# Performance work log

Measured on AMD Instinct MI355X. Metric: run time of the kernel, lower is better.

## Reference

```python
import jax, jax.numpy as jnp
import numpy as np

B, S, IN, D, H, L, DFF, C = 64, 256, 32, 512, 8, 2, 2048, 16
DH = D // H


def setup_inputs() -> dict:
    key = jax.random.key(0)
    ks = iter(jax.random.split(key, 40))
    r = lambda shp, s=0.02: (jax.random.normal(next(ks), shp, dtype=jnp.float32) * s)
    inp = {
        'x': jax.random.normal(next(ks), (B, S, IN), dtype=jnp.float32),
        'W_emb': r((IN, D)), 'b_emb': jnp.zeros((D,), jnp.float32),
        'Wq': r((L, D, D)), 'bq': jnp.zeros((L, D), jnp.float32),
        'Wk': r((L, D, D)), 'bk': jnp.zeros((L, D), jnp.float32),
        'Wv': r((L, D, D)), 'bv': jnp.zeros((L, D), jnp.float32),
        'Wo': r((L, D, D)), 'bo': jnp.zeros((L, D), jnp.float32),
        'ln1_s': jnp.ones((L, D), jnp.float32), 'ln1_b': jnp.zeros((L, D), jnp.float32),
        'W1': r((L, D, DFF)), 'b1': jnp.zeros((L, DFF), jnp.float32),
        'W2': r((L, DFF, D)), 'b2': jnp.zeros((L, D), jnp.float32),
        'ln2_s': jnp.ones((L, D), jnp.float32), 'ln2_b': jnp.zeros((L, D), jnp.float32),
        'e1_w': r((D, 128)), 'e1_b': jnp.zeros((128,), jnp.float32),
        'e2_w': r((128, D)), 'e2_b': jnp.zeros((D,), jnp.float32),
        'd1_w': r((D, 128)), 'd1_b': jnp.zeros((128,), jnp.float32),
        'd2_w': r((128, D)), 'd2_b': jnp.zeros((D,), jnp.float32),
        'y': jax.random.randint(next(ks), (B, S, 1), 0, C, dtype=jnp.int32),
    }
    return inp


def _ln(x, s, b):
    m = x.mean(-1, keepdims=True)
    v = ((x - m) ** 2).mean(-1, keepdims=True)
    return (x - m) / jnp.sqrt(v + 1e-5) * s + b


def _ari(a, t, n_cls):
    # adjusted rand index from contingency matrix (labels in [0, n_cls))
    idx = a * n_cls + t
    cm = jnp.zeros((n_cls * n_cls,), jnp.float32).at[idx].add(1.0).reshape(n_cls, n_cls)
    comb2 = lambda m: m * (m - 1.0) * 0.5
    sij = comb2(cm).sum()
    sa = comb2(cm.sum(1)).sum()
    sb = comb2(cm.sum(0)).sum()
    n = jnp.float32(a.shape[0])
    exp = sa * sb / (n * (n - 1.0) * 0.5)
    mx = 0.5 * (sa + sb)
    return (sij - exp) / (mx - exp)


def _net(x, W_emb, b_emb, Wq, bq, Wk, bk, Wv, bv, Wo, bo, ln1_s, ln1_b,
         W1, b1, W2, b2, ln2_s, ln2_b, e1_w, e1_b, e2_w, e2_b, d1_w, d1_b, d2_w, d2_b):
    h = x @ W_emb + b_emb  # [B,S,D]
    for l in range(L):
        q = (h @ Wq[l] + bq[l]).reshape(B, S, H, DH)
        k = (h @ Wk[l] + bk[l]).reshape(B, S, H, DH)
        v = (h @ Wv[l] + bv[l]).reshape(B, S, H, DH)
        scores = jnp.einsum('bqhd,bkhd->bhqk', q, k) / jnp.sqrt(jnp.float32(DH))
        attn = jax.nn.softmax(scores, axis=-1)
        o = jnp.einsum('bhqk,bkhd->bqhd', attn, v).reshape(B, S, D)
        h = _ln(h + o @ Wo[l] + bo[l], ln1_s[l], ln1_b[l])
        f = jax.nn.relu(h @ W1[l] + b1[l]) @ W2[l] + b2[l]
        h = _ln(h + f, ln2_s[l], ln2_b[l])
    enc = jax.nn.relu(h @ e1_w + e1_b) @ e2_w + e2_b
    z = jax.nn.relu(enc @ d1_w + d1_b) @ d2_w + d2_b  # input_to_cluster [B,S,D]
    return z


def reference(x, W_emb, b_emb, Wq, bq, Wk, bk, Wv, bv, Wo, bo, ln1_s, ln1_b,
              W1, b1, W2, b2, ln2_s, ln2_b, e1_w, e1_b, e2_w, e2_b,
              d1_w, d1_b, d2_w, d2_b, y):
    z = _net(x, W_emb, b_emb, Wq, bq, Wk, bk, Wv, bv, Wo, bo, ln1_s, ln1_b,
             W1, b1, W2, b2, ln2_s, ln2_b, e1_w, e1_b, e2_w, e2_b, d1_w, d1_b, d2_w, d2_b)
    # pairwise squared distances across batch per timestep: [S,B,B]
    sq = jnp.sum(z * z, -1)                       # [B,S]
    gram = jnp.einsum('bsd,csd->sbc', z, z)       # [S,B,B]
    dist = sq.T[:, :, None] + sq.T[:, None, :] - 2.0 * gram
    p = jax.nn.softmax(-dist, axis=-1)
    _, knn = jax.lax.top_k(p, C)                  # [S,B,C]
    # tot_sum: rows of dist selected once per i where knn[s,b,i]==i
    counts = jnp.sum(knn == jnp.arange(C)[None, None, :], axis=-1)  # [S,B]
    tot_sum = jnp.sum(dist.sum(-1) * counts.astype(dist.dtype))
    # gather neighbor labels and take mode (ties -> smallest value, like torch.mode)
    y2 = y[..., 0]                                 # [B,S]
    labels = y2[knn, jnp.arange(S)[:, None, None]] # [S,B,C]
    cnt = jnp.sum(labels[..., None] == jnp.arange(C), axis=-2)      # [S,B,C]
    assigned = jnp.argmax(cnt, axis=-1).astype(jnp.int32).reshape(-1)  # S*B (row-major, as torch)
    y_true = y.reshape(-1)                         # B*S (as torch: mismatched order is faithful)
    ari = _ari(assigned, y_true, C)
    return tot_sum, ari, assigned, z
```

## Files before the change

kernel.cpp:

```cpp
#include <hip/hip_runtime.h>
#include <cstdint>
#include <cmath>

#define B_ 64
#define S_ 256
#define IN_ 32
#define D_ 512
#define H_ 8
#define L_ 2
#define DFF_ 2048
#define C_ 16
#define DH_ 64
#define NTOK (B_*S_)
#define HALF_ 8192

typedef __attribute__((ext_vector_type(8))) short bf16x8;
typedef __attribute__((ext_vector_type(4))) float f32x4;
typedef __attribute__((ext_vector_type(8))) ushort ushortx8;

__device__ __forceinline__ ushort bf16_rn(float x) {
    union { float f; uint32_t u; } v; v.f = x;
    uint32_t r = v.u + 0x7fffu + ((v.u >> 16) & 1u);
    return (ushort)(r >> 16);
}
__device__ __forceinline__ float bf16_f32(ushort h) {
    union { uint32_t u; float f; } v; v.u = ((uint32_t)h) << 16;
    return v.f;
}

#define GLDS(gp, lp) __builtin_amdgcn_global_load_lds( \
    (const __attribute__((address_space(1))) void*)(gp), \
    (__attribute__((address_space(3))) void*)(lp), 16, 0, 0)

__device__ __forceinline__ int xcd_swz(int lid, int nwg) {
    return (lid & 7) * (nwg >> 3) + (lid >> 3);
}

template<int MODE>
__global__ __launch_bounds__(256)
void gemm3(const ushort* __restrict__ Ahi, const ushort* __restrict__ Alo,
           const ushort* __restrict__ Bhi, const ushort* __restrict__ Blo,
           const float* __restrict__ bias,
           float* __restrict__ Cf, ushort* __restrict__ Chi, ushort* __restrict__ Clo,
           int M, int N, int K)
{
    __shared__ __align__(16) ushort Als[2][2][128*32];
    __shared__ __align__(16) ushort Bls[2][2][128*32];
    const int tid  = threadIdx.x;
    const int wave = tid >> 6, lane = tid & 63;
    const int nwg = gridDim.x * gridDim.y;
    const int swz = xcd_swz(blockIdx.y * gridDim.x + blockIdx.x, nwg);
    const int m0 = (swz / gridDim.x) << 7, n0 = (swz % gridDim.x) << 7;
    const int wr = wave >> 1, wc = wave & 1;

    const ushort* Ah = Ahi + (size_t)m0 * K;
    const ushort* Al = Alo + (size_t)m0 * K;
    const ushort* Bh = Bhi + (size_t)n0 * K;
    const ushort* Bl = Blo + (size_t)n0 * K;

    const int KT = K >> 5;

    f32x4 acc[4][4];
    #pragma unroll
    for (int m = 0; m < 4; ++m)
        #pragma unroll
        for (int n = 0; n < 4; ++n)
            acc[m][n] = (f32x4){0.f, 0.f, 0.f, 0.f};

    auto stage = [&](int buf, int kk) {
        #pragma unroll
        for (int i = 0; i < 2; ++i) {
            const int rbase = wave * 32 + i * 16;
            const int row   = rbase + (lane >> 2);
            const int slot  = (lane & 3) ^ ((row >> 1) & 3);
            GLDS(Ah + (size_t)row * K + kk + slot * 8, &Als[buf][0][rbase * 32]);
            GLDS(Al + (size_t)row * K + kk + slot * 8, &Als[buf][1][rbase * 32]);
            GLDS(Bh + (size_t)row * K + kk + slot * 8, &Bls[buf][0][rbase * 32]);
            GLDS(Bl + (size_t)row * K + kk + slot * 8, &Bls[buf][1][rbase * 32]);
        }
    };

    stage(0, 0);
    for (int t = 0; t < KT; ++t) {
        const int buf = t & 1;
        if (t + 1 < KT) {
            stage(buf ^ 1, (t + 1) << 5);
            asm volatile("s_waitcnt vmcnt(8)" ::: "memory");
        } else {
            asm volatile("s_waitcnt vmcnt(0)" ::: "memory");
        }
        __builtin_amdgcn_sched_barrier(0);
        __builtin_amdgcn_s_barrier();

        const int chunk = lane >> 4;
        bf16x8 afh[4], afl[4], bfh[4], bfl[4];
        #pragma unroll
        for (int m = 0; m < 4; ++m) {
            const int row = wr * 64 + m * 16 + (lane & 15);
            const int sl  = chunk ^ ((row >> 1) & 3);
            afh[m] = *(const bf16x8*)(&Als[buf][0][row * 32 + sl * 8]);
            afl[m] = *(const bf16x8*)(&Als[buf][1][row * 32 + sl * 8]);
        }
        #pragma unroll
        for (int n = 0; n < 4; ++n) {
            const int row = wc * 64 + n * 16 + (lane & 15);
            const int sl  = chunk ^ ((row >> 1) & 3);
            bfh[n] = *(const bf16x8*)(&Bls[buf][0][row * 32 + sl * 8]);
            bfl[n] = *(const bf16x8*)(&Bls[buf][1][row * 32 + sl * 8]);
        }
        #pragma unroll
        for (int m = 0; m < 4; ++m)
            #pragma unroll
            for (int n = 0; n < 4; ++n) {
                acc[m][n] = __builtin_amdgcn_mfma_f32_16x16x32_bf16(afh[m], bfh[n], acc[m][n], 0, 0, 0);
                acc[m][n] = __builtin_amdgcn_mfma_f32_16x16x32_bf16(afh[m], bfl[n], acc[m][n], 0, 0, 0);
                acc[m][n] = __builtin_amdgcn_mfma_f32_16x16x32_bf16(afl[m], bfh[n], acc[m][n], 0, 0, 0);
            }
        __builtin_amdgcn_sched_barrier(0);
        __builtin_amdgcn_s_barrier();
    }

    const int col_l = lane & 15;
    float bv[4];
    #pragma unroll
    for (int n = 0; n < 4; ++n) bv[n] = bias[n0 + wc * 64 + n * 16 + col_l];
    #pragma unroll
    for (int m = 0; m < 4; ++m) {
        #pragma unroll
        for (int j = 0; j < 4; ++j) {
            const size_t grow = (size_t)(m0 + wr * 64 + m * 16 + (lane >> 4) * 4 + j);
            #pragma unroll
            for (int n = 0; n < 4; ++n) {
                float x = acc[m][n][j] + bv[n];
                if (MODE & 1) x = fmaxf(x, 0.f);
                const size_t gidx = grow * N + (n0 + wc * 64 + n * 16 + col_l);
                if (MODE < 2) {
                    Cf[gidx] = x;
                } else {
                    ushort hb = bf16_rn(x);
                    Chi[gidx] = hb;
                    Clo[gidx] = bf16_rn(x - bf16_f32(hb));
                }
            }
        }
    }
}

__global__ __launch_bounds__(256)
void qks_gemm(const ushort* __restrict__ qkvhi, const ushort* __restrict__ qkvlo,
              ushort* __restrict__ Phi, ushort* __restrict__ Plo,
              ushort* __restrict__ VThi, ushort* __restrict__ VTlo)
{
    __shared__ __align__(16) ushort Qls[2][128*64];
    __shared__ __align__(16) ushort Kls[2][128*64];
    const int tid = threadIdx.x, wave = tid >> 6, lane = tid & 63;
    const int swz = xcd_swz(blockIdx.y * 2 + blockIdx.x, 256);
    const int bh = swz >> 1, qt = swz & 1;
    const int b = bh >> 3, h = bh & 7;

    const ushort* Qh = qkvhi + ((size_t)(b * 256 + qt * 128)) * 1536 + h * 64;
    const ushort* Ql = qkvlo + ((size_t)(b * 256 + qt * 128)) * 1536 + h * 64;
    const ushort* Kh = qkvhi + ((size_t)(b * 256)) * 1536 + 512 + h * 64;
    const ushort* Kl = qkvlo + ((size_t)(b * 256)) * 1536 + 512 + h * 64;

    auto stage128 = [&](const ushort* src, ushort* dst) {
        #pragma unroll
        for (int j = 0; j < 4; ++j) {
            const int rl   = j * 32 + wave * 8 + (lane >> 3);
            const int slot = (lane & 7) ^ (rl & 7);
            GLDS(src + (size_t)rl * 1536 + slot * 8, dst + (j * 32 + wave * 8) * 64);
        }
    };

    f32x4 acc[2][16];
    #pragma unroll
    for (int mi = 0; mi < 2; ++mi)
        #pragma unroll
        for (int nj = 0; nj < 16; ++nj)
            acc[mi][nj] = (f32x4){0.f, 0.f, 0.f, 0.f};

    stage128(Qh, &Qls[0][0]);
    stage128(Ql, &Qls[1][0]);
    stage128(Kh, &Kls[0][0]);
    stage128(Kl, &Kls[1][0]);
    asm volatile("s_waitcnt vmcnt(0)" ::: "memory");
    __builtin_amdgcn_sched_barrier(0);
    __builtin_amdgcn_s_barrier();

    bf16x8 qh[2][2], ql[2][2];
    #pragma unroll
    for (int mi = 0; mi < 2; ++mi)
        #pragma unroll
        for (int ks = 0; ks < 2; ++ks) {
            const int row = wave * 32 + mi * 16 + (lane & 15);
            const int es  = (ks * 4 + (lane >> 4)) ^ (lane & 7);
            qh[mi][ks] = *(const bf16x8*)&Qls[0][row * 64 + es * 8];
            ql[mi][ks] = *(const bf16x8*)&Qls[1][row * 64 + es * 8];
        }

    #pragma unroll
    for (int hk = 0; hk < 2; ++hk) {
        if (hk == 1) {
            __syncthreads();
            stage128(Kh + (size_t)128 * 1536, &Kls[0][0]);
            stage128(Kl + (size_t)128 * 1536, &Kls[1][0]);
            asm volatile("s_waitcnt vmcnt(0)" ::: "memory");
            __builtin_amdgcn_sched_barrier(0);
            __builtin_amdgcn_s_barrier();
        }
        #pragma unroll
        for (int ng = 0; ng < 2; ++ng) {
            bf16x8 kh[4][2], kl[4][2];
            #pragma unroll
            for (int nj = 0; nj < 4; ++nj)
                #pragma unroll
                for (int ks = 0; ks < 2; ++ks) {
                    const int row = (ng * 4 + nj) * 16 + (lane & 15);
                    const int es  = (ks * 4 + (lane >> 4)) ^ (lane & 7);
                    kh[nj][ks] = *(const bf16x8*)&Kls[0][row * 64 + es * 8];
                    kl[nj][ks] = *(const bf16x8*)&Kls[1][row * 64 + es * 8];
                }
            #pragma unroll
            for (int mi = 0; mi < 2; ++mi)
                #pragma unroll
                for (int nj = 0; nj < 4; ++nj) {
                    const int an = hk * 8 + ng * 4 + nj;
                    #pragma unroll
                    for (int ks = 0; ks < 2; ++ks) {
                        acc[mi][an] = __builtin_amdgcn_mfma_f32_16x16x32_bf16(qh[mi][ks], kh[nj][ks], acc[mi][an], 0, 0, 0);
                        acc[mi][an] = __builtin_amdgcn_mfma_f32_16x16x32_bf16(qh[mi][ks], kl[nj][ks], acc[mi][an], 0, 0, 0);
                        acc[mi][an] = __builtin_amdgcn_mfma_f32_16x16x32_bf16(ql[mi][ks], kh[nj][ks], acc[mi][an], 0, 0, 0);
                    }
                }
        }
    }

    const int colb = lane & 15;
    #pragma unroll
    for (int mi = 0; mi < 2; ++mi) {
        #pragma unroll
        for (int j = 0; j < 4; ++j) {
            float v[16];
            float mx = -INFINITY;
            #pragma unroll
            for (int nj = 0; nj < 16; ++nj) {
                v[nj] = acc[mi][nj][j] * 0.125f;
                mx = fmaxf(mx, v[nj]);
            }
            #pragma unroll
            for (int d = 1; d < 16; d <<= 1) mx = fmaxf(mx, __shfl_xor(mx, d));
            float sum = 0.f;
            #pragma unroll
            for (int nj = 0; nj < 16; ++nj) {
                v[nj] = expf(v[nj] - mx);
                sum += v[nj];
            }
            #pragma unroll
            for (int d = 1; d < 16; d <<= 1) sum += __shfl_xor(sum, d);
            const float inv = 1.0f / sum;
            const int qrow = qt * 128 + wave * 32 + mi * 16 + (lane >> 4) * 4 + j;
            const size_t base = ((size_t)bh * 256 + qrow) * 256;
            #pragma unroll
            for (int nj = 0; nj < 16; ++nj) {
                float p = v[nj] * inv;
                ushort hb = bf16_rn(p);
                Phi[base + nj * 16 + colb] = hb;
                Plo[base + nj * 16 + colb] = bf16_rn(p - bf16_f32(hb));
            }
        }
    }

    {
        ushort* T = &Qls[0][0];
        const int TP = 144;
        const ushort* vsrcs[2] = {
            qkvhi + ((size_t)(b * 256 + qt * 128)) * 1536 + 1024 + h * 64,
            qkvlo + ((size_t)(b * 256 + qt * 128)) * 1536 + 1024 + h * 64 };
        ushort* vdsts[2] = { VThi, VTlo };
        #pragma unroll
        for (int pass = 0; pass < 2; ++pass) {
            __syncthreads();
            if (tid < 128) {
                const ushort* p = vsrcs[pass] + (size_t)tid * 1536;
                #pragma unroll
                for (int i = 0; i < 8; ++i) {
                    ushortx8 vv = *(const ushortx8*)(p + i * 8);
                    #pragma unroll
                    for (int j = 0; j < 8; ++j) T[(i * 8 + j) * TP + tid] = vv[j];
                }
            }
            __syncthreads();
            {
                const int dh = tid >> 2;
                const int kseg = (tid & 3) * 32;
                ushort* op = vdsts[pass] + ((size_t)bh * 64 + dh) * 256 + qt * 128 + kseg;
                #pragma unroll
                for (int i = 0; i < 4; ++i) {
                    ushortx8 vv;
                    #pragma unroll
                    for (int j = 0; j < 8; ++j) vv[j] = T[dh * TP + kseg + i * 8 + j];
                    *(ushortx8*)(op + i * 8) = vv;
                }
            }
        }
    }
}

__global__ __launch_bounds__(256)
void pv_gemm(const ushort* __restrict__ Phi, const ushort* __restrict__ Plo,
             const ushort* __restrict__ VThi, const ushort* __restrict__ VTlo,
             ushort* __restrict__ obhi, ushort* __restrict__ oblo, int t0)
{
    __shared__ __align__(16) ushort Als[2][2][128*32];
    __shared__ __align__(16) ushort Bls[2][2][64*32];
    const int tid = threadIdx.x, wave = tid >> 6, lane = tid & 63;
    const int swz = xcd_swz(blockIdx.y * 2 + blockIdx.x, 256);
    const int bh = swz >> 1, qt = swz & 1;
    const ushort* Ah = Phi + ((size_t)bh * 256 + qt * 128) * 256;
    const ushort* Al = Plo + ((size_t)bh * 256 + qt * 128) * 256;
    const ushort* Bh = VThi + (size_t)bh * 64 * 256;
    const ushort* Bl = VTlo + (size_t)bh * 64 * 256;

    f32x4 acc[2][4];
    #pragma unroll
    for (int m = 0; m < 2; ++m)
        #pragma unroll
        for (int n = 0; n < 4; ++n)
            acc[m][n] = (f32x4){0.f, 0.f, 0.f, 0.f};

    auto stage = [&](int buf, int kk) {
        #pragma unroll
        for (int i = 0; i < 2; ++i) {
            const int rbase = wave * 32 + i * 16;
            const int row   = rbase + (lane >> 2);
            const int slot  = (lane & 3) ^ ((row >> 1) & 3);
            GLDS(Ah + (size_t)row * 256 + kk + slot * 8, &Als[buf][0][rbase * 32]);
            GLDS(Al + (size_t)row * 256 + kk + slot * 8, &Als[buf][1][rbase * 32]);
        }
        const int rbase2 = wave * 16;
        const int row2   = rbase2 + (lane >> 2);
        const int slot2  = (lane & 3) ^ ((row2 >> 1) & 3);
        GLDS(Bh + (size_t)row2 * 256 + kk + slot2 * 8, &Bls[buf][0][rbase2 * 32]);
        GLDS(Bl + (size_t)row2 * 256 + kk + slot2 * 8, &Bls[buf][1][rbase2 * 32]);
    };

    stage(0, 0);
    for (int t = 0; t < 8; ++t) {
        const int buf = t & 1;
        __syncthreads();
        if (t < 7) stage(buf ^ 1, (t + 1) << 5);
        const int chunk = lane >> 4;
        bf16x8 afh[2], afl[2], bfh[4], bfl[4];
        #pragma unroll
        for (int m = 0; m < 2; ++m) {
            const int row = wave * 32 + m * 16 + (lane & 15);
            const int sl  = chunk ^ ((row >> 1) & 3);
            afh[m] = *(const bf16x8*)(&Als[buf][0][row * 32 + sl * 8]);
            afl[m] = *(const bf16x8*)(&Als[buf][1][row * 32 + sl * 8]);
        }
        #pragma unroll
        for (int n = 0; n < 4; ++n) {
            const int row = n * 16 + (lane & 15);
            const int sl  = chunk ^ ((row >> 1) & 3);
            bfh[n] = *(const bf16x8*)(&Bls[buf][0][row * 32 + sl * 8]);
            bfl[n] = *(const bf16x8*)(&Bls[buf][1][row * 32 + sl * 8]);
        }
        #pragma unroll
        for (int m = 0; m < 2; ++m)
            #pragma unroll
            for (int n = 0; n < 4; ++n) {
                acc[m][n] = __builtin_amdgcn_mfma_f32_16x16x32_bf16(afh[m], bfh[n], acc[m][n], 0, 0, 0);
                acc[m][n] = __builtin_amdgcn_mfma_f32_16x16x32_bf16(afh[m], bfl[n], acc[m][n], 0, 0, 0);
                acc[m][n] = __builtin_amdgcn_mfma_f32_16x16x32_bf16(afl[m], bfh[n], acc[m][n], 0, 0, 0);
            }
        __syncthreads();
    }

    const int b = bh >> 3, h = bh & 7;
    const int col_l = lane & 15;
    #pragma unroll
    for (int m = 0; m < 2; ++m)
        #pragma unroll
        for (int j = 0; j < 4; ++j) {
            const int q = qt * 128 + wave * 32 + m * 16 + (lane >> 4) * 4 + j;
            const size_t token = (size_t)t0 + (size_t)b * 256 + q;
            #pragma unroll
            for (int n = 0; n < 4; ++n) {
                const int col = h * 64 + n * 16 + col_l;
                float x = acc[m][n][j];
                ushort hb = bf16_rn(x);
                obhi[token * 512 + col] = hb;
                oblo[token * 512 + col] = bf16_rn(x - bf16_f32(hb));
            }
        }
}

__global__ __launch_bounds__(256)
void gemm_f32(const float* __restrict__ A, const float* __restrict__ W,
              const float* __restrict__ bias, float* __restrict__ Cc,
              ushort* __restrict__ Chi, ushort* __restrict__ Clo,
              int M, int N, int K)
{
    __shared__ float As[16][68];
    __shared__ float Bs[16][64];
    const int tid = threadIdx.x;
    const int tx = tid & 15, ty = tid >> 4;
    const int m0 = blockIdx.y << 6, n0 = blockIdx.x << 6;
    const int arow = tid >> 2, ak4 = (tid & 3) << 2;
    const int brow = tid >> 4, bc4 = (tid & 15) << 2;
    float acc[4][4] = {};
    const float* aptr = A + (size_t)(m0 + arow) * K + ak4;
    const float* bptr = W + (size_t)brow * N + n0 + bc4;
    for (int k0 = 0; k0 < K; k0 += 16) {
        float4 av = *(const float4*)(aptr + k0);
        float4 bv = *(const float4*)(bptr + (size_t)k0 * N);
        __syncthreads();
        As[ak4+0][arow] = av.x; As[ak4+1][arow] = av.y;
        As[ak4+2][arow] = av.z; As[ak4+3][arow] = av.w;
        *(float4*)&Bs[brow][bc4] = bv;
        __syncthreads();
        #pragma unroll
        for (int kk = 0; kk < 16; ++kk) {
            float4 a = *(const float4*)&As[kk][ty << 2];
            float4 b = *(const float4*)&Bs[kk][tx << 2];
            float ar[4] = {a.x,a.y,a.z,a.w};
            float br[4] = {b.x,b.y,b.z,b.w};
            #pragma unroll
            for (int i = 0; i < 4; ++i)
                #pragma unroll
                for (int j = 0; j < 4; ++j)
                    acc[i][j] = fmaf(ar[i], br[j], acc[i][j]);
        }
    }
    float4 bb = *(const float4*)(bias + n0 + (tx << 2));
    #pragma unroll
    for (int i = 0; i < 4; ++i) {
        int m = m0 + (ty << 2) + i;
        float o[4];
        o[0] = acc[i][0] + bb.x; o[1] = acc[i][1] + bb.y;
        o[2] = acc[i][2] + bb.z; o[3] = acc[i][3] + bb.w;
        ushort4 hh, ll;
        hh.x = bf16_rn(o[0]); ll.x = bf16_rn(o[0] - bf16_f32(hh.x));
        hh.y = bf16_rn(o[1]); ll.y = bf16_rn(o[1] - bf16_f32(hh.y));
        hh.z = bf16_rn(o[2]); ll.z = bf16_rn(o[2] - bf16_f32(hh.z));
        hh.w = bf16_rn(o[3]); ll.w = bf16_rn(o[3] - bf16_f32(hh.w));
        const size_t base = (size_t)m * N + n0 + (tx << 2);
        *(float4*)(Cc + base) = (float4){o[0],o[1],o[2],o[3]};
        *(ushort4*)(Chi + base) = hh;
        *(ushort4*)(Clo + base) = ll;
    }
}

__global__ __launch_bounds__(256)
void prep_layer(const float* __restrict__ Wq, const float* __restrict__ Wk,
                const float* __restrict__ Wv, const float* __restrict__ Wo,
                const float* __restrict__ W1, const float* __restrict__ W2,
                const float* __restrict__ bq, const float* __restrict__ bk,
                const float* __restrict__ bv,
                ushort* __restrict__ WTQKV_HI, ushort* __restrict__ WTQKV_LO,
                ushort* __restrict__ WTO_HI, ushort* __restrict__ WTO_LO,
                ushort* __restrict__ WT1_HI, ushort* __restrict__ WT1_LO,
                ushort* __restrict__ WT2_HI, ushort* __restrict__ WT2_LO,
                float* __restrict__ biasqkv)
{
    __shared__ float T[64][65];
    const int blk = blockIdx.x;
    const int tid = threadIdx.x;
    if (blk >= 768) {
        int i = (blk - 768) * 256 + tid;
        biasqkv[i] = (i < 512) ? bq[i] : (i < 1024 ? bk[i - 512] : bv[i - 1024]);
        return;
    }
    const float* W; ushort* Thi; ushort* Tlo; int K, N, bx, by;
    if (blk < 192) {
        const int wsel = blk / 64, idx = blk % 64;
        W = (wsel == 0) ? Wq : ((wsel == 1) ? Wk : Wv);
        Thi = WTQKV_HI + (size_t)wsel * 512 * 512;
        Tlo = WTQKV_LO + (size_t)wsel * 512 * 512;
        K = 512; N = 512; bx = idx % 8; by = idx / 8;
    } else if (blk < 256) {
        const int idx = blk - 192;
        W = Wo; Thi = WTO_HI; Tlo = WTO_LO;
        K = 512; N = 512; bx = idx % 8; by = idx / 8;
    } else if (blk < 512) {
        const int idx = blk - 256;
        W = W1; Thi = WT1_HI; Tlo = WT1_LO;
        K = 512; N = 2048; bx = idx % 32; by = idx / 32;
    } else {
        const int idx = blk - 512;
        W = W2; Thi = WT2_HI; Tlo = WT2_LO;
        K = 2048; N = 512; bx = idx % 8; by = idx / 8;
    }
    const int k0 = by << 6, n0 = bx << 6;
    #pragma unroll
    for (int i = 0; i < 16; ++i) {
        int idx = tid + i * 256;
        int kl = idx >> 6, nl = idx & 63;
        T[nl][kl] = W[(size_t)(k0 + kl) * N + n0 + nl];
    }
    __syncthreads();
    #pragma unroll
    for (int i = 0; i < 16; ++i) {
        int idx = tid + i * 256;
        int nl = idx >> 6, kl = idx & 63;
        float x = T[nl][kl];
        ushort hb = bf16_rn(x);
        size_t o = (size_t)(n0 + nl) * K + k0 + kl;
        Thi[o] = hb;
        Tlo[o] = bf16_rn(x - bf16_f32(hb));
    }
}

__global__ __launch_bounds__(256)
void transpose_split(const float* __restrict__ W, ushort* __restrict__ Thi,
                     ushort* __restrict__ Tlo, int K, int N)
{
    __shared__ float T[64][65];
    const int k0 = blockIdx.y << 6, n0 = blockIdx.x << 6;
    const int tid = threadIdx.x;
    #pragma unroll
    for (int i = 0; i < 16; ++i) {
        int idx = tid + i * 256;
        int kl = idx >> 6, nl = idx & 63;
        T[nl][kl] = W[(size_t)(k0 + kl) * N + n0 + nl];
    }
    __syncthreads();
    #pragma unroll
    for (int i = 0; i < 16; ++i) {
        int idx = tid + i * 256;
        int nl = idx >> 6, kl = idx & 63;
        float x = T[nl][kl];
        ushort hb = bf16_rn(x);
        size_t o = (size_t)(n0 + nl) * K + k0 + kl;
        Thi[o] = hb;
        Tlo[o] = bf16_rn(x - bf16_f32(hb));
    }
}

__global__ __launch_bounds__(256)
void ln_res(float* __restrict__ h, const float* __restrict__ t,
            const float* __restrict__ sc, const float* __restrict__ bi,
            ushort* __restrict__ hhi, ushort* __restrict__ hlo)
{
    const int row = blockIdx.x * 4 + (threadIdx.x >> 6);
    const int lane = threadIdx.x & 63;
    const size_t off = (size_t)row * D_ + (size_t)lane * 8;
    float x[8];
    float4 a0 = *(const float4*)(h + off),  a1 = *(const float4*)(h + off + 4);
    float4 b0 = *(const float4*)(t + off),  b1 = *(const float4*)(t + off + 4);
    x[0]=a0.x+b0.x; x[1]=a0.y+b0.y; x[2]=a0.z+b0.z; x[3]=a0.w+b0.w;
    x[4]=a1.x+b1.x; x[5]=a1.y+b1.y; x[6]=a1.z+b1.z; x[7]=a1.w+b1.w;

    float s = 0.f;
    #pragma unroll
    for (int i = 0; i < 8; ++i) s += x[i];
    #pragma unroll
    for (int d = 1; d < 64; d <<= 1) s += __shfl_xor(s, d);
    float mean = s * (1.0f / 512.0f);

    float vsum = 0.f;
    #pragma unroll
    for (int i = 0; i < 8; ++i) { float dx = x[i] - mean; vsum += dx * dx; }
    #pragma unroll
    for (int d = 1; d < 64; d <<= 1) vsum += __shfl_xor(vsum, d);
    float den = sqrtf(vsum * (1.0f / 512.0f) + 1e-5f);

    float4 s0 = *(const float4*)(sc + lane*8), s1 = *(const float4*)(sc + lane*8 + 4);
    float4 c0 = *(const float4*)(bi + lane*8), c1 = *(const float4*)(bi + lane*8 + 4);
    float scv[8] = {s0.x,s0.y,s0.z,s0.w,s1.x,s1.y,s1.z,s1.w};
    float biv[8] = {c0.x,c0.y,c0.z,c0.w,c1.x,c1.y,c1.z,c1.w};
    float out[8];
    ushort hh[8], ll[8];
    #pragma unroll
    for (int i = 0; i < 8; ++i) {
        out[i] = (x[i] - mean) / den * scv[i] + biv[i];
        hh[i] = bf16_rn(out[i]);
        ll[i] = bf16_rn(out[i] - bf16_f32(hh[i]));
    }
    *(float4*)(h + off)     = (float4){out[0],out[1],out[2],out[3]};
    *(float4*)(h + off + 4) = (float4){out[4],out[5],out[6],out[7]};
    *(ushort4*)(hhi + off)     = (ushort4){hh[0],hh[1],hh[2],hh[3]};
    *(ushort4*)(hhi + off + 4) = (ushort4){hh[4],hh[5],hh[6],hh[7]};
    *(ushort4*)(hlo + off)     = (ushort4){ll[0],ll[1],ll[2],ll[3]};
    *(ushort4*)(hlo + off + 4) = (ushort4){ll[4],ll[5],ll[6],ll[7]};
}

__global__ __launch_bounds__(256)
void zout_sq(const float* __restrict__ z, float* __restrict__ outz,
             float* __restrict__ sq)
{
#pragma clang fp contract(off)
    const int row = blockIdx.x * 4 + (threadIdx.x >> 6);
    const int lane = threadIdx.x & 63;
    const size_t off = (size_t)row * D_ + (size_t)lane * 8;
    const float* p = z + off;
    float4 a0 = *(const float4*)(p), a1 = *(const float4*)(p + 4);
    float vv[8] = {a0.x,a0.y,a0.z,a0.w,a1.x,a1.y,a1.z,a1.w};
    float* op = outz + off;
    #pragma unroll
    for (int i = 0; i < 8; ++i) op[i] = vv[i];
    float s = 0.f;
    #pragma unroll
    for (int i = 0; i < 8; ++i) { float t = vv[i] * vv[i]; s = s + t; }
    #pragma unroll
    for (int d = 1; d < 64; d <<= 1) s += __shfl_xor(s, d);
    if (lane == 0) sq[row] = s;
}

__global__ __launch_bounds__(256)
void gram_kernel(const float* __restrict__ z, float* __restrict__ gram)
{
    __shared__ float Ls[16][68];
    const int s = blockIdx.x;
    const int tid = threadIdx.x;
    const int tx = tid & 15, ty = tid >> 4;
    const int arow = tid >> 2, ak4 = (tid & 3) << 2;
    float acc[4][4] = {};
    const float* zp = z + ((size_t)arow * S_ + s) * D_ + ak4;
    for (int k0 = 0; k0 < D_; k0 += 16) {
        float4 av = *(const float4*)(zp + k0);
        __syncthreads();
        Ls[ak4+0][arow] = av.x; Ls[ak4+1][arow] = av.y;
        Ls[ak4+2][arow] = av.z; Ls[ak4+3][arow] = av.w;
        __syncthreads();
        #pragma unroll
        for (int kk = 0; kk < 16; ++kk) {
            float4 a = *(const float4*)&Ls[kk][ty << 2];
            float4 b = *(const float4*)&Ls[kk][tx << 2];
            float ar[4] = {a.x,a.y,a.z,a.w};
            float br[4] = {b.x,b.y,b.z,b.w};
            #pragma unroll
            for (int i = 0; i < 4; ++i)
                #pragma unroll
                for (int j = 0; j < 4; ++j)
                    acc[i][j] = fmaf(ar[i], br[j], acc[i][j]);
        }
    }
    #pragma unroll
    for (int i = 0; i < 4; ++i) {
        float4 o = {acc[i][0], acc[i][1], acc[i][2], acc[i][3]};
        *(float4*)(gram + ((size_t)s * 64 + (ty<<2) + i) * 64 + (tx<<2)) = o;
    }
}

__global__ __launch_bounds__(64)
void cluster_kernel(const float* __restrict__ gram, const float* __restrict__ sq,
                    const int* __restrict__ y, float* __restrict__ contrib,
                    int* __restrict__ assigned, float* __restrict__ out_assigned_f)
{
#pragma clang fp contract(off)
    __shared__ float G[64][65];
    __shared__ float sqs[64];
    const int s = blockIdx.x, b = threadIdx.x;
    for (int i = b; i < 4096; i += 64)
        G[i >> 6][i & 63] = gram[(size_t)s * 4096 + i];
    sqs[b] = sq[(size_t)b * S_ + s];
    __syncthreads();

    const float sqb = sqs[b];
    float dmin = INFINITY, dsum = 0.f;
    for (int c = 0; c < 64; ++c) {
        float d = sqb + sqs[c] - 2.0f * G[b][c];
        dmin = fminf(dmin, d);
        dsum = dsum + d;
    }
    float Z = 0.f;
    for (int c = 0; c < 64; ++c) {
        float d = sqb + sqs[c] - 2.0f * G[b][c];
        float e = expf(dmin - d);
        G[b][c] = e;
        Z = Z + e;
    }
    for (int c = 0; c < 64; ++c) G[b][c] = G[b][c] / Z;

    int knn[16];
    #pragma unroll
    for (int j = 0; j < 16; ++j) {
        float bp = -1.f; int bi2 = 0;
        for (int c = 0; c < 64; ++c) {
            float pv = G[b][c];
            if (pv > bp) { bp = pv; bi2 = c; }
        }
        knn[j] = bi2;
        G[b][bi2] = -1.f;
    }
    int cmatch = 0;
    #pragma unroll
    for (int j = 0; j < 16; ++j) cmatch += (knn[j] == j) ? 1 : 0;
    int lab[16];
    #pragma unroll
    for (int j = 0; j < 16; ++j) lab[j] = y[knn[j] * S_ + s];
    int bestc = -1, bestcls = 0;
    #pragma unroll
    for (int cls = 0; cls < 16; ++cls) {
        int cc = 0;
        #pragma unroll
        for (int j = 0; j < 16; ++j) cc += (lab[j] == cls) ? 1 : 0;
        if (cc > bestc) { bestc = cc; bestcls = cls; }
    }
    const int oi = s * 64 + b;
    contrib[oi] = dsum * (float)cmatch;
    assigned[oi] = bestcls;
    out_assigned_f[oi] = (float)bestcls;
}

__global__ __launch_bounds__(256)
void finalize_kernel(const float* __restrict__ contrib, const int* __restrict__ assigned,
                     const int* __restrict__ y, float* __restrict__ dout)
{
#pragma clang fp contract(off)
    __shared__ int cm[256];
    __shared__ float red[256];
    const int tid = threadIdx.x;
    cm[tid] = 0;
    float s = 0.f;
    for (int i = tid; i < NTOK; i += 256) s = s + contrib[i];
    red[tid] = s;
    __syncthreads();
    for (int i = tid; i < NTOK; i += 256)
        atomicAdd(&cm[assigned[i] * 16 + y[i]], 1);
    __syncthreads();
    for (int st = 128; st > 0; st >>= 1) {
        if (tid < st) red[tid] = red[tid] + red[tid + st];
        __syncthreads();
    }
    if (tid == 0) {
        dout[0] = red[0];
        float sij = 0.f, sa = 0.f, sb = 0.f;
        for (int i = 0; i < 256; ++i) {
            float mm = (float)cm[i];
            sij = sij + mm * (mm - 1.0f) * 0.5f;
        }
        for (int r = 0; r < 16; ++r) {
            int rs = 0;
            for (int c2 = 0; c2 < 16; ++c2) rs += cm[r * 16 + c2];
            float mm = (float)rs;
            sa = sa + mm * (mm - 1.0f) * 0.5f;
        }
        for (int c2 = 0; c2 < 16; ++c2) {
            int cs = 0;
            for (int r = 0; r < 16; ++r) cs += cm[r * 16 + c2];
            float mm = (float)cs;
            sb = sb + mm * (mm - 1.0f) * 0.5f;
        }
        float n = 16384.0f;
        float expv = sa * sb / (n * (n - 1.0f) * 0.5f);
        float mx = 0.5f * (sa + sb);
        dout[1] = (sij - expv) / (mx - expv);
    }
}

extern "C" void kernel_launch(void* const* d_in, const int* in_sizes, int n_in,
                              void* d_out, int out_size, void* d_ws, size_t ws_size,
                              hipStream_t stream)
{
    (void)in_sizes; (void)n_in; (void)out_size; (void)ws_size;
    const float* x     = (const float*)d_in[0];
    const float* W_emb = (const float*)d_in[1];
    const float* b_emb = (const float*)d_in[2];
    const float* Wq    = (const float*)d_in[3];
    const float* bq    = (const float*)d_in[4];
    const float* Wk    = (const float*)d_in[5];
    const float* bk    = (const float*)d_in[6];
    const float* Wv    = (const float*)d_in[7];
    const float* bv    = (const float*)d_in[8];
    const float* Wo    = (const float*)d_in[9];
    const float* bo    = (const float*)d_in[10];
    const float* ln1_s = (const float*)d_in[11];
    const float* ln1_b = (const float*)d_in[12];
    const float* W1    = (const float*)d_in[13];
    const float* b1    = (const float*)d_in[14];
    const float* W2    = (const float*)d_in[15];
    const float* b2    = (const float*)d_in[16];
    const float* ln2_s = (const float*)d_in[17];
    const float* ln2_b = (const float*)d_in[18];
    const float* e1_w  = (const float*)d_in[19];
    const float* e1_b  = (const float*)d_in[20];
    const float* e2_w  = (const float*)d_in[21];
    const float* e2_b  = (const float*)d_in[22];
    const float* d1_w  = (const float*)d_in[23];
    const float* d1_b  = (const float*)d_in[24];
    const float* d2_w  = (const float*)d_in[25];
    const float* d2_b  = (const float*)d_in[26];
    const int*   y     = (const int*)d_in[27];

    float* ws = (float*)d_ws;
    float*  h    = ws;
    ushort* hhi  = (ushort*)(ws + 8388608);
    ushort* hlo  = (ushort*)(ws + 12582912);
    float*  SCR  = ws + 16777216;
    ushort* obhi = (ushort*)(ws + 37748736);
    ushort* oblo = (ushort*)(ws + 41943040);
    float*  wt   = ws + 46137344;
    ushort* WTQKV_HI = (ushort*)wt;
    ushort* WTQKV_LO = WTQKV_HI + 786432;
    ushort* WTO_HI   = WTQKV_LO + 786432;
    ushort* WTO_LO   = WTO_HI + 262144;
    ushort* WT1_HI   = WTO_LO + 262144;
    ushort* WT1_LO   = WT1_HI + 1048576;
    ushort* WT2_HI   = WT1_LO + 1048576;
    ushort* WT2_LO   = WT2_HI + 1048576;
    ushort* WE1_HI   = WT2_LO + 1048576;
    ushort* WE1_LO   = WE1_HI + 65536;
    ushort* WE2_HI   = WE1_LO + 65536;
    ushort* WE2_LO   = WE2_HI + 65536;
    ushort* WD1_HI   = WE2_LO + 65536;
    ushort* WD1_LO   = WD1_HI + 65536;
    ushort* WD2_HI   = WD1_LO + 65536;
    ushort* WD2_LO   = WD2_HI + 65536;
    float*  biasqkv  = ws + 49545216;

    ushort* Phi_  = (ushort*)SCR;
    ushort* Plo_  = (ushort*)(SCR + 4194304);
    ushort* qkvhi = (ushort*)(SCR + 8388608);
    ushort* qkvlo = (ushort*)(SCR + 11534336);
    ushort* VThi  = (ushort*)(SCR + 14680064);
    ushort* VTlo  = (ushort*)(SCR + 15728640);
    float*  Of32  = SCR;
    ushort* f1hi  = (ushort*)SCR;
    ushort* f1lo  = (ushort*)(SCR + 8388608);
    float*  Xhalf = SCR + 16777216;
    ushort* enchi = (ushort*)SCR;
    ushort* enclo = (ushort*)(SCR + 4194304);
    float*  z     = SCR + 8388608;
    float*  gram  = SCR + 16777216;
    float*  sqb_  = SCR + 17825792;
    float*  contrib = SCR + 17842176;
    int*    assigned = (int*)(SCR + 17858560);
    ushort* t1hi = obhi;
    ushort* t1lo = oblo;
    ushort* t2hi = obhi + 2097152;
    ushort* t2lo = oblo + 2097152;
    float*  dout = (float*)d_out;

    dim3 blk(256);
    auto gg = [](int M, int N) { return dim3(N >> 7, M >> 7); };

    transpose_split<<<dim3(2, 8), blk, 0, stream>>>(e1_w, WE1_HI, WE1_LO, 512, 128);
    transpose_split<<<dim3(8, 2), blk, 0, stream>>>(e2_w, WE2_HI, WE2_LO, 128, 512);
    transpose_split<<<dim3(2, 8), blk, 0, stream>>>(d1_w, WD1_HI, WD1_LO, 512, 128);
    transpose_split<<<dim3(8, 2), blk, 0, stream>>>(d2_w, WD2_HI, WD2_LO, 128, 512);

    gemm_f32<<<dim3(8, 256), blk, 0, stream>>>(x, W_emb, b_emb, h, hhi, hlo, NTOK, D_, IN_);

    for (int l = 0; l < L_; ++l) {
        prep_layer<<<dim3(774), blk, 0, stream>>>(
            Wq + (size_t)l*D_*D_, Wk + (size_t)l*D_*D_, Wv + (size_t)l*D_*D_,
            Wo + (size_t)l*D_*D_, W1 + (size_t)l*D_*DFF_, W2 + (size_t)l*DFF_*D_,
            bq + l*D_, bk + l*D_, bv + l*D_,
            WTQKV_HI, WTQKV_LO, WTO_HI, WTO_LO, WT1_HI, WT1_LO, WT2_HI, WT2_LO,
            biasqkv);

        for (int qtr = 0; qtr < 4; ++qtr) {
            const size_t hoff = (size_t)qtr * 4096 * 512;
            gemm3<2><<<gg(4096, 1536), blk, 0, stream>>>(
                hhi + hoff, hlo + hoff, WTQKV_HI, WTQKV_LO, biasqkv,
                nullptr, qkvhi, qkvlo, 4096, 1536, 512);
            qks_gemm<<<dim3(2, 128), blk, 0, stream>>>(qkvhi, qkvlo, Phi_, Plo_,
                                                       VThi, VTlo);
            pv_gemm<<<dim3(2, 128), blk, 0, stream>>>(Phi_, Plo_, VThi, VTlo,
                                                      obhi, oblo, qtr * 4096);
        }
        gemm3<0><<<gg(NTOK, 512), blk, 0, stream>>>(
            obhi, oblo, WTO_HI, WTO_LO, bo + l*D_,
            Of32, nullptr, nullptr, NTOK, 512, 512);
        ln_res<<<dim3(NTOK / 4), blk, 0, stream>>>(h, Of32, ln1_s + l*D_, ln1_b + l*D_, hhi, hlo);

        for (int half = 0; half < 2; ++half) {
            const size_t ro = (size_t)half * HALF_ * D_;
            gemm3<3><<<gg(HALF_, DFF_), blk, 0, stream>>>(
                hhi + ro, hlo + ro, WT1_HI, WT1_LO, b1 + l*DFF_,
                nullptr, f1hi, f1lo, HALF_, 2048, 512);
            gemm3<0><<<gg(HALF_, 512), blk, 0, stream>>>(
                f1hi, f1lo, WT2_HI, WT2_LO, b2 + l*D_,
                Xhalf, nullptr, nullptr, HALF_, 512, 2048);
            ln_res<<<dim3(HALF_ / 4), blk, 0, stream>>>(
                h + ro, Xhalf, ln2_s + l*D_, ln2_b + l*D_, hhi + ro, hlo + ro);
        }
    }

    gemm3<3><<<gg(NTOK, 128), blk, 0, stream>>>(
        hhi, hlo, WE1_HI, WE1_LO, e1_b, nullptr, t1hi, t1lo, NTOK, 128, 512);
    gemm3<2><<<gg(NTOK, 512), blk, 0, stream>>>(
        t1hi, t1lo, WE2_HI, WE2_LO, e2_b, nullptr, enchi, enclo, NTOK, 512, 128);
    gemm3<3><<<gg(NTOK, 128), blk, 0, stream>>>(
        enchi, enclo, WD1_HI, WD1_LO, d1_b, nullptr, t2hi, t2lo, NTOK, 128, 512);
    gemm3<0><<<gg(NTOK, 512), blk, 0, stream>>>(
        t2hi, t2lo, WD2_HI, WD2_LO, d2_b, z, nullptr, nullptr, NTOK, 512, 128);

    zout_sq<<<dim3(NTOK / 4), blk, 0, stream>>>(z, dout + 16386, sqb_);
    gram_kernel<<<dim3(S_), blk, 0, stream>>>(z, gram);
    cluster_kernel<<<dim3(S_), dim3(64), 0, stream>>>(gram, sqb_, y, contrib, assigned, dout + 2);
    finalize_kernel<<<dim3(1), blk, 0, stream>>>(contrib, assigned, y, dout);
}
```

Baseline: 1.441 ms.

## Group GEMM tile mapping per XCD and add 64-row kernel for N=128

Replaces the GEMM block-to-tile swizzle with a grouped mapping: each XCD gets a contiguous M range and walks N in groups, to improve L2 reuse of A and B tiles. Adds a dedicated 64x128-tile split-bf16 GEMM for the two N=128, K=512 encoder/decoder layers, launching 256 blocks instead of 128 to fill more CUs. The mapping assumes specific grid shapes divisible by the group sizes.

```diff
diff --git a/kernel.cpp b/kernel.cpp
--- a/kernel.cpp
+++ b/kernel.cpp
@@ -48,9 +48,17 @@
     __shared__ __align__(16) ushort Bls[2][2][128*32];
     const int tid  = threadIdx.x;
     const int wave = tid >> 6, lane = tid & 63;
-    const int nwg = gridDim.x * gridDim.y;
-    const int swz = xcd_swz(blockIdx.y * gridDim.x + blockIdx.x, nwg);
-    const int m0 = (swz / gridDim.x) << 7, n0 = (swz % gridDim.x) << 7;
+    const int gx = gridDim.x;
+    const int nwg = gx * gridDim.y;
+    const int lid = blockIdx.y * gx + blockIdx.x;
+    const int xcd = lid & 7, l = lid >> 3;
+    const int nl  = nwg >> 3;
+    const int GN  = (gx <= 8) ? gx : ((gx == 16) ? 8 : 6);
+    const int cm  = nl / gx;
+    const int seg = l / (cm * GN);
+    const int r   = l - seg * (cm * GN);
+    const int m0 = (xcd * cm + r / GN) << 7;
+    const int n0 = (seg * GN + r % GN) << 7;
     const int wr = wave >> 1, wc = wave & 1;
 
     const ushort* Ah = Ahi + (size_t)m0 * K;
@@ -141,6 +149,107 @@
                     Chi[gidx] = hb;
                     Clo[gidx] = bf16_rn(x - bf16_f32(hb));
                 }
+            }
+        }
+    }
+}
+
+__global__ __launch_bounds__(256)
+void gemm3_n128(const ushort* __restrict__ Ahi, const ushort* __restrict__ Alo,
+                const ushort* __restrict__ Bhi, const ushort* __restrict__ Blo,
+                const float* __restrict__ bias,
+                ushort* __restrict__ Chi, ushort* __restrict__ Clo, int M)
+{
+    __shared__ __align__(16) ushort Als[2][2][64*32];
+    __shared__ __align__(16) ushort Bls[2][2][128*32];
+    const int tid = threadIdx.x, wave = tid >> 6, lane = tid & 63;
+    const int m0 = xcd_swz(blockIdx.x, gridDim.x) << 6;
+    const int K = 512, N = 128;
+
+    const ushort* Ah = Ahi + (size_t)m0 * K;
+    const ushort* Al = Alo + (size_t)m0 * K;
+
+    f32x4 acc[4][2];
+    #pragma unroll
+    for (int m = 0; m < 4; ++m)
+        #pragma unroll
+        for (int n = 0; n < 2; ++n)
+            acc[m][n] = (f32x4){0.f, 0.f, 0.f, 0.f};
+
+    auto stage = [&](int buf, int kk) {
+        {
+            const int rbase = wave * 16;
+            const int row   = rbase + (lane >> 2);
+            const int slot  = (lane & 3) ^ ((row >> 1) & 3);
+            GLDS(Ah + (size_t)row * K + kk + slot * 8, &Als[buf][0][rbase * 32]);
+            GLDS(Al + (size_t)row * K + kk + slot * 8, &Als[buf][1][rbase * 32]);
+        }
+        #pragma unroll
+        for (int i = 0; i < 2; ++i) {
+            const int rbase = wave * 32 + i * 16;
+            const int row   = rbase + (lane >> 2);
+            const int slot  = (lane & 3) ^ ((row >> 1) & 3);
+            GLDS(Bhi + (size_t)row * K + kk + slot * 8, &Bls[buf][0][rbase * 32]);
+            GLDS(Blo + (size_t)row * K + kk + slot * 8, &Bls[buf][1][rbase * 32]);
+        }
+    };
+
+    stage(0, 0);
+    for (int t = 0; t < 16; ++t) {
+        const int buf = t & 1;
+        if (t + 1 < 16) {
+            stage(buf ^ 1, (t + 1) << 5);
+            asm volatile("s_waitcnt vmcnt(6)" ::: "memory");
+        } else {
+            asm volatile("s_waitcnt vmcnt(0)" ::: "memory");
+        }
+        __builtin_amdgcn_sched_barrier(0);
+        __builtin_amdgcn_s_barrier();
+
+        const int chunk = lane >> 4;
+        bf16x8 afh[4], afl[4], bfh[2], bfl[2];
+        #pragma unroll
+        for (int m = 0; m < 4; ++m) {
+            const int row = m * 16 + (lane & 15);
+            const int sl  = chunk ^ ((row >> 1) & 3);
+            afh[m] = *(const bf16x8*)(&Als[buf][0][row * 32 + sl * 8]);
+            afl[m] = *(const bf16x8*)(&Als[buf][1][row * 32 + sl * 8]);
+        }
+        #pragma unroll
+        for (int n = 0; n < 2; ++n) {
+            const int row = wave * 32 + n * 16 + (lane & 15);
+            const int sl  = chunk ^ ((row >> 1) & 3);
+            bfh[n] = *(const bf16x8*)(&Bls[buf][0][row * 32 + sl * 8]);
+            bfl[n] = *(const bf16x8*)(&Bls[buf][1][row * 32 + sl * 8]);
+        }
+        #pragma unroll
+        for (int m = 0; m < 4; ++m)
+            #pragma unroll
+            for (int n = 0; n < 2; ++n) {
+                acc[m][n] = __builtin_amdgcn_mfma_f32_16x16x32_bf16(afh[m], bfh[n], acc[m][n], 0, 0, 0);
+                acc[m][n] = __builtin_amdgcn_mfma_f32_16x16x32_bf16(afh[m], bfl[n], acc[m][n], 0, 0, 0);
+                acc[m][n] = __builtin_amdgcn_mfma_f32_16x16x32_bf16(afl[m], bfh[n], acc[m][n], 0, 0, 0);
+            }
+        __builtin_amdgcn_sched_barrier(0);
+        __builtin_amdgcn_s_barrier();
+    }
+
+    const int col_l = lane & 15;
+    float bv[2];
+    #pragma unroll
+    for (int n = 0; n < 2; ++n) bv[n] = bias[wave * 32 + n * 16 + col_l];
+    #pragma unroll
+    for (int m = 0; m < 4; ++m) {
+        #pragma unroll
+        for (int j = 0; j < 4; ++j) {
+            const size_t grow = (size_t)(m0 + m * 16 + (lane >> 4) * 4 + j);
+            #pragma unroll
+            for (int n = 0; n < 2; ++n) {
+                float x = fmaxf(acc[m][n][j] + bv[n], 0.f);
+                const size_t gidx = grow * N + (wave * 32 + n * 16 + col_l);
+                ushort hb = bf16_rn(x);
+                Chi[gidx] = hb;
+                Clo[gidx] = bf16_rn(x - bf16_f32(hb));
             }
         }
     }
@@ -879,12 +988,12 @@
         }
     }
 
-    gemm3<3><<<gg(NTOK, 128), blk, 0, stream>>>(
-        hhi, hlo, WE1_HI, WE1_LO, e1_b, nullptr, t1hi, t1lo, NTOK, 128, 512);
+    gemm3_n128<<<dim3(256), blk, 0, stream>>>(
+        hhi, hlo, WE1_HI, WE1_LO, e1_b, t1hi, t1lo, NTOK);
     gemm3<2><<<gg(NTOK, 512), blk, 0, stream>>>(
         t1hi, t1lo, WE2_HI, WE2_LO, e2_b, nullptr, enchi, enclo, NTOK, 512, 128);
-    gemm3<3><<<gg(NTOK, 128), blk, 0, stream>>>(
-        enchi, enclo, WD1_HI, WD1_LO, d1_b, nullptr, t2hi, t2lo, NTOK, 128, 512);
+    gemm3_n128<<<dim3(256), blk, 0, stream>>>(
+        enchi, enclo, WD1_HI, WD1_LO, d1_b, t2hi, t2lo, NTOK);
     gemm3<0><<<gg(NTOK, 512), blk, 0, stream>>>(
         t2hi, t2lo, WD2_HI, WD2_LO, d2_b, z, nullptr, nullptr, NTOK, 512, 128);
 
```

After: 1.439 ms. Within noise of the previous version (-0.1%).
